# Performance work log

Measured on AMD Instinct MI355X. Metric: run time of the kernel, lower is better.

The kernel has to match this reference:

```python
import jax, jax.numpy as jnp
import numpy as np

WS = 7   # window_size
SS = 3   # shift_size
NH = 6   # num_heads
EPS = 1e-5


def _partition(x, ws):
    # [b,h,w,c] -> [b*(h//ws)*(w//ws), ws*ws, c]
    b, h, w, c = x.shape
    x = x.reshape(b, h // ws, ws, w // ws, ws, c)
    return x.transpose(0, 1, 3, 2, 4, 5).reshape(-1, ws * ws, c)


def _reverse(windows, ws, h, w, b):
    c = windows.shape[-1]
    x = windows.reshape(b, h // ws, w // ws, ws, ws, c)
    return x.transpose(0, 1, 3, 2, 4, 5).reshape(b, h, w, c)


def _make_mask(h, w, ws, ss):
    # static (numpy) shifted-window attention mask, [nw, ws*ws, ws*ws]
    img = np.zeros((h, w), dtype=np.float32)
    slices = (slice(0, -ws), slice(-ws, -ss), slice(-ss, None))
    cnt = 0
    for hs in slices:
        for wsl in slices:
            img[hs, wsl] = cnt
            cnt += 1
    mw = img.reshape(h // ws, ws, w // ws, ws).transpose(0, 2, 1, 3).reshape(-1, ws * ws)
    am = mw[:, None, :] - mw[:, :, None]
    mask = np.where(am != 0, -100.0, 0.0).astype(np.float32)
    return jnp.asarray(mask)


def _layernorm(x, g, b):
    mu = jnp.mean(x, axis=-1, keepdims=True)
    var = jnp.var(x, axis=-1, keepdims=True)
    return (x - mu) * jax.lax.rsqrt(var + EPS) * g + b


def setup_inputs() -> dict:
    key = jax.random.key(0)
    ks = jax.random.split(key, 8)
    dim = 192
    s = lambda fan: 1.0 / np.sqrt(fan)
    return {
        "x": jax.random.normal(ks[0], (64, 56, 56, dim), dtype=jnp.float32),
        "n1_g": jnp.ones((dim,), jnp.float32),
        "n1_b": jnp.zeros((dim,), jnp.float32),
        "qkv_w": jax.random.normal(ks[1], (dim, 3 * dim), jnp.float32) * s(dim),
        "qkv_b": jnp.zeros((3 * dim,), jnp.float32),
        "proj_w": jax.random.normal(ks[2], (dim, dim), jnp.float32) * s(dim),
        "proj_b": jnp.zeros((dim,), jnp.float32),
        "n2_g": jnp.ones((dim,), jnp.float32),
        "n2_b": jnp.zeros((dim,), jnp.float32),
        "w1": jax.random.normal(ks[3], (dim, 4 * dim), jnp.float32) * s(dim),
        "b1": jnp.zeros((4 * dim,), jnp.float32),
        "w2": jax.random.normal(ks[4], (4 * dim, dim), jnp.float32) * s(4 * dim),
        "b2": jnp.zeros((dim,), jnp.float32),
    }


def reference(x, n1_g, n1_b, qkv_w, qkv_b, proj_w, proj_b, n2_g, n2_b, w1, b1, w2, b2):
    b, h, w, c = x.shape
    hd = c // NH
    scale = hd ** -0.5

    sc = x
    xn = _layernorm(x, n1_g, n1_b)
    sx = jnp.roll(xn, shift=(-SS, -SS), axis=(1, 2))

    xw = _partition(sx, WS)                      # [B_, n, c], n = WS*WS
    B_, n, _ = xw.shape

    qkv = xw @ qkv_w + qkv_b                      # [B_, n, 3c]
    qkv = qkv.reshape(B_, n, 3, NH, hd).transpose(2, 0, 3, 1, 4)
    q, k, v = qkv[0], qkv[1], qkv[2]              # [B_, NH, n, hd]

    attn = jnp.einsum("whnd,whmd->whnm", q, k) * scale   # [B_, NH, n, n]
    mask = _make_mask(h, w, WS, SS)               # [nw, n, n]
    nw = mask.shape[0]
    attn = attn.reshape(b // nw * 1 if False else b, nw, NH, n, n) if False else attn.reshape(B_ // nw, nw, NH, n, n)
    attn = attn + mask[None, :, None, :, :]
    attn = attn.reshape(-1, NH, n, n)
    attn = jax.nn.softmax(attn, axis=-1)

    out = jnp.einsum("whnm,whmd->whnd", attn, v)  # [B_, NH, n, hd]
    out = out.transpose(0, 2, 1, 3).reshape(B_, n, c)
    out = out @ proj_w + proj_b

    sx = _reverse(out, WS, h, w, b)
    xs = jnp.roll(sx, shift=(SS, SS), axis=(1, 2))

    x2 = sc + xs
    x2n = _layernorm(x2, n2_g, n2_b)
    mlp = jax.nn.gelu(x2n @ w1 + b1, approximate=False) @ w2 + b2
    return x2 + mlp
```

## Files before the change

kernel.cpp:

```cpp
#include <hip/hip_runtime.h>

typedef __attribute__((ext_vector_type(4))) float f32x4;
typedef __attribute__((ext_vector_type(8))) short bf16x8;

#define NHEAD 6

__device__ __forceinline__ unsigned short f2bf(float f){
  union{float f;unsigned int u;}c; c.f=f;
  unsigned int x=c.u;
  return (unsigned short)((x + 0x7FFFu + ((x>>16)&1u)) >> 16);
}
__device__ __forceinline__ unsigned int pack2(float a, float b){
  return (unsigned int)f2bf(a) | ((unsigned int)f2bf(b)<<16);
}

__global__ void wt_kernel(const float* __restrict__ w, unsigned short* __restrict__ wt,
                          int K, int N){
  int idx = blockIdx.x*256 + threadIdx.x;
  if (idx >= K*N) return;
  int k = idx / N, n = idx - k*N;
  wt[(size_t)n*K + k] = f2bf(w[idx]);
}

template<int SHIFT>
__global__ __launch_bounds__(256) void ln_kernel(const float* __restrict__ x,
    const float* __restrict__ gw, const float* __restrict__ bw,
    unsigned short* __restrict__ out){
  int tok  = blockIdx.x*4 + (threadIdx.x>>6);
  int lane = threadIdx.x & 63;
  const float* row = x + (size_t)tok*192;
  float4 v = make_float4(0.f,0.f,0.f,0.f);
  if (lane < 48) v = *(const float4*)(row + lane*4);
  float s  = v.x+v.y+v.z+v.w;
  float s2 = v.x*v.x+v.y*v.y+v.z*v.z+v.w*v.w;
  #pragma unroll
  for (int off=32; off; off>>=1){ s += __shfl_xor(s,off); s2 += __shfl_xor(s2,off); }
  float mu = s*(1.f/192.f);
  float rs = rsqrtf(s2*(1.f/192.f) - mu*mu + 1e-5f);
  size_t otok;
  if (SHIFT){
    int b = tok/3136; int hw = tok - b*3136; int h = hw/56; int w = hw - h*56;
    int hs = h-3; if (hs<0) hs += 56;
    int wsh = w-3; if (wsh<0) wsh += 56;
    int wr = hs/7, r = hs - wr*7, wc = wsh/7, c = wsh - wc*7;
    otok = ((size_t)b*64 + wr*8 + wc)*49 + r*7 + c;
  } else {
    otok = (size_t)tok;
  }
  if (lane < 48){
    int cb = lane*4;
    ushort4 o;
    o.x = f2bf((v.x-mu)*rs*gw[cb+0] + bw[cb+0]);
    o.y = f2bf((v.y-mu)*rs*gw[cb+1] + bw[cb+1]);
    o.z = f2bf((v.z-mu)*rs*gw[cb+2] + bw[cb+2]);
    o.w = f2bf((v.w-mu)*rs*gw[cb+3] + bw[cb+3]);
    *(ushort4*)(out + otok*192 + cb) = o;
  }
}

enum { EPI_QKV=0, EPI_PROJ=1, EPI_GELU=2, EPI_FINAL=3 };

template<int EPI>
__global__ __launch_bounds__(256) void gemm_kernel(
    const unsigned short* __restrict__ A,
    const unsigned short* __restrict__ BT,
    const float* __restrict__ bias,
    const float* __restrict__ res,
    void* __restrict__ Cout,
    int M, int N, int K)
{
  __shared__ unsigned short lA[128*64];
  __shared__ unsigned short lB[64*64];
  const int tid  = threadIdx.x;
  const int wave = tid>>6, lane = tid&63;
  const int wm = wave>>1, wn = wave&1;
  const int lr = lane&15, lh = lane>>4;
  const int m0 = blockIdx.y*128, n0 = blockIdx.x*64;

  f32x4 zero = {0.f,0.f,0.f,0.f};
  f32x4 acc[4][2];
  #pragma unroll
  for (int i=0;i<4;i++){ acc[i][0]=zero; acc[i][1]=zero; }

  const int row8 = tid>>3, col8 = (tid&7)*8;
  const unsigned short* Ag = A  + (size_t)(m0 + row8)*K + col8;
  const unsigned short* Bg = BT + (size_t)(n0 + row8)*K + col8;

  for (int kt=0; kt<K; kt+=64){
    __syncthreads();
    #pragma unroll
    for (int i=0;i<4;i++){
      __builtin_amdgcn_global_load_lds(
        (const __attribute__((address_space(1))) void*)(Ag + (size_t)i*32*K + kt),
        (__attribute__((address_space(3))) void*)(lA + (i*256 + wave*64)*8),
        16, 0, 0);
    }
    #pragma unroll
    for (int i=0;i<2;i++){
      __builtin_amdgcn_global_load_lds(
        (const __attribute__((address_space(1))) void*)(Bg + (size_t)i*32*K + kt),
        (__attribute__((address_space(3))) void*)(lB + (i*256 + wave*64)*8),
        16, 0, 0);
    }
    __syncthreads();

    bf16x8 af[4][2], bfv[2][2];
    #pragma unroll
    for (int mi=0;mi<4;mi++)
      #pragma unroll
      for (int ks=0;ks<2;ks++)
        af[mi][ks] = *(const bf16x8*)&lA[(wm*64+mi*16+lr)*64 + ks*32 + lh*8];
    #pragma unroll
    for (int ni=0;ni<2;ni++)
      #pragma unroll
      for (int ks=0;ks<2;ks++)
        bfv[ni][ks] = *(const bf16x8*)&lB[(wn*32+ni*16+lr)*64 + ks*32 + lh*8];
    #pragma unroll
    for (int mi=0;mi<4;mi++)
      #pragma unroll
      for (int ni=0;ni<2;ni++)
        #pragma unroll
        for (int ks=0;ks<2;ks++)
          acc[mi][ni] = __builtin_amdgcn_mfma_f32_16x16x32_bf16(
              af[mi][ks], bfv[ni][ks], acc[mi][ni], 0,0,0);
  }

  #pragma unroll
  for (int mi=0;mi<4;mi++){
    #pragma unroll
    for (int ni=0;ni<2;ni++){
      int col = n0 + wn*32 + ni*16 + lr;
      float bv = bias[col];
      #pragma unroll
      for (int r=0;r<4;r++){
        int row = m0 + wm*64 + mi*16 + lh*4 + r;
        float v = acc[mi][ni][r] + bv;
        if (EPI == EPI_QKV){
          int win = row/49; int n = row - win*49;
          int which = col/192; int rem = col - which*192;
          int head = rem>>5, d = rem&31;
          size_t idx = (size_t)win*28224 + (size_t)which*9408 + head*1568 + n*32 + d;
          ((unsigned short*)Cout)[idx] = f2bf(v);
        } else if (EPI == EPI_GELU){
          float g = 0.5f*v*(1.0f + erff(v*0.70710678118654752f));
          ((unsigned short*)Cout)[(size_t)row*N + col] = f2bf(g);
        } else if (EPI == EPI_FINAL){
          size_t idx = (size_t)row*N + col;
          ((float*)Cout)[idx] = res[idx] + v;
        } else {
          int win = row/49; int nn = row - win*49;
          int b  = win>>6; int wi = win&63; int wr = wi>>3; int wc = wi&7;
          int r7 = nn/7;  int c7 = nn - r7*7;
          int h = wr*7 + r7 + 3; if (h>=56) h-=56;
          int w = wc*7 + c7 + 3; if (w>=56) w-=56;
          size_t idx = (((size_t)b*3136) + h*56 + w)*192 + col;
          ((float*)Cout)[idx] = res[idx] + v;
        }
      }
    }
  }
}

__global__ __launch_bounds__(256) void attn_kernel(const unsigned short* __restrict__ qkv,
                                                   unsigned short* __restrict__ aout){
  __shared__ __align__(16) unsigned short ldsQK[4][4096];
  __shared__ __align__(16) unsigned short ldsV[4][2048];
  const int wave = threadIdx.x>>6, lane = threadIdx.x&63;
  const int lr = lane&15, lh = lane>>4;
  const int unit = blockIdx.x*4 + wave;
  const int win  = unit/NHEAD, head = unit - win*NHEAD;

  unsigned short* Q  = ldsQK[wave];
  unsigned short* Kl = ldsQK[wave] + 2048;
  unsigned short* P  = ldsQK[wave];
  unsigned short* Vt = ldsV[wave];

  const size_t wbase = (size_t)win*28224 + (size_t)head*1568;
  const unsigned short* gQ = qkv + wbase;
  const unsigned short* gK = qkv + wbase + 9408;
  const unsigned short* gV = qkv + wbase + 18816;

  {
    uint4 z = make_uint4(0,0,0,0);
    #pragma unroll
    for (int i=0;i<4;i++) *(uint4*)&Vt[(i*64+lane)*8] = z;
  }

  #pragma unroll
  for (int i=0;i<4;i++){
    int idx = i*64 + lane;
    if (idx < 196){
      int row = idx>>2, blk = idx&3;
      int sb = (blk ^ (row&3) ^ ((row>>2)&3));
      uint4 dq = *(const uint4*)(gQ + idx*8);
      *(uint4*)&Q[row*32 + sb*8] = dq;
      uint4 dk = *(const uint4*)(gK + idx*8);
      *(uint4*)&Kl[row*32 + sb*8] = dk;
    }
  }
  #pragma unroll
  for (int i=0;i<4;i++){
    int idx = i*64 + lane;
    if (idx < 196){
      int row = idx>>2, d0 = (idx&3)*8;
      uint4 dv = *(const uint4*)(gV + idx*8);
      unsigned int wds[4] = {dv.x, dv.y, dv.z, dv.w};
      int rb = row>>3, re = row&7;
      #pragma unroll
      for (int j=0;j<8;j++){
        unsigned short t = (unsigned short)(wds[j>>1] >> ((j&1)*16));
        Vt[(d0+j)*64 + ((rb ^ j)*8) + re] = t;
      }
    }
  }

  bf16x8 kf[4], qf[4];
  #pragma unroll
  for (int t=0;t<4;t++){
    int row = t*16 + lr;
    int off = row*32 + ((lh ^ (row&3) ^ ((row>>2)&3))*8);
    kf[t] = *(const bf16x8*)&Kl[off];
    qf[t] = *(const bf16x8*)&Q[off];
  }

  f32x4 zero = {0.f,0.f,0.f,0.f};
  f32x4 S[4][4];
  #pragma unroll
  for (int mi=0;mi<4;mi++)
    #pragma unroll
    for (int ni=0;ni<4;ni++)
      S[mi][ni] = __builtin_amdgcn_mfma_f32_16x16x32_bf16(kf[mi], qf[ni], zero, 0,0,0);

  const int wi = win & 63, wr = wi>>3, wc = wi&7;
  const bool hasmask = (wr==7) || (wc==7);
  const float scale = 0.17677669529663687f;

  #pragma unroll
  for (int ni=0;ni<4;ni++){
    int q = ni*16 + lr;
    int idq = 0;
    if (hasmask){
      int qr = q/7, qc = q - qr*7;
      int ih = (wr==7) ? ((qr>=4)?2:1) : 0;
      int iw = (wc==7) ? ((qc>=4)?2:1) : 0;
      idq = ih*3 + iw;
    }
    #pragma unroll
    for (int mi=0;mi<4;mi++){
      #pragma unroll
      for (int r=0;r<4;r++){
        int key = mi*16 + lh*4 + r;
        float s;
        if (key >= 49) s = -1e30f;
        else {
          float add = 0.f;
          if (hasmask){
            int kr = key/7, kc = key - kr*7;
            int ih = (wr==7) ? ((kr>=4)?2:1) : 0;
            int iw = (wc==7) ? ((kc>=4)?2:1) : 0;
            add = ((ih*3+iw) == idq) ? 0.f : -100.f;
          }
          s = S[mi][ni][r]*scale + add;
        }
        S[mi][ni][r] = s;
      }
    }
    float m = -1e30f;
    #pragma unroll
    for (int mi=0;mi<4;mi++)
      #pragma unroll
      for (int r=0;r<4;r++) m = fmaxf(m, S[mi][ni][r]);
    m = fmaxf(m, __shfl_xor(m, 16));
    m = fmaxf(m, __shfl_xor(m, 32));
    float sum = 0.f;
    #pragma unroll
    for (int mi=0;mi<4;mi++)
      #pragma unroll
      for (int r=0;r<4;r++){
        float p = __expf(S[mi][ni][r] - m);
        S[mi][ni][r] = p; sum += p;
      }
    sum += __shfl_xor(sum, 16);
    sum += __shfl_xor(sum, 32);
    float inv = 1.f/sum;
    #pragma unroll
    for (int mi=0;mi<4;mi++){
      int keyb = mi*16 + lh*4;
      int blk = keyb>>3, e0 = keyb&7;
      int addr = q*64 + ((blk ^ (q&7))*8) + e0;
      *(unsigned int*)&P[addr]   = pack2(S[mi][ni][0]*inv, S[mi][ni][1]*inv);
      *(unsigned int*)&P[addr+2] = pack2(S[mi][ni][2]*inv, S[mi][ni][3]*inv);
    }
  }

  bf16x8 vf[2][2];
  #pragma unroll
  for (int mt=0;mt<2;mt++)
    #pragma unroll
    for (int ks=0;ks<2;ks++){
      int row = mt*16 + lr;
      vf[mt][ks] = *(const bf16x8*)&Vt[row*64 + (((ks*4+lh) ^ (row&7))*8)];
    }
  f32x4 O[2][4];
  #pragma unroll
  for (int ni=0;ni<4;ni++){
    int q = ni*16 + lr;
    bf16x8 pf0 = *(const bf16x8*)&P[q*64 + (((0*4+lh) ^ (q&7))*8)];
    bf16x8 pf1 = *(const bf16x8*)&P[q*64 + (((1*4+lh) ^ (q&7))*8)];
    #pragma unroll
    for (int mt=0;mt<2;mt++){
      f32x4 t = __builtin_amdgcn_mfma_f32_16x16x32_bf16(vf[mt][0], pf0, zero, 0,0,0);
      O[mt][ni] = __builtin_amdgcn_mfma_f32_16x16x32_bf16(vf[mt][1], pf1, t, 0,0,0);
    }
  }

  #pragma unroll
  for (int ni=0;ni<4;ni++){
    int q = ni*16 + lr;
    if (q < 49){
      size_t ob = ((size_t)win*49 + q)*192 + head*32 + lh*4;
      #pragma unroll
      for (int mt=0;mt<2;mt++){
        *(unsigned int*)(aout + ob + mt*16)     = pack2(O[mt][ni][0], O[mt][ni][1]);
        *(unsigned int*)(aout + ob + mt*16 + 2) = pack2(O[mt][ni][2], O[mt][ni][3]);
      }
    }
  }
}

extern "C" void kernel_launch(void* const* d_in, const int* in_sizes, int n_in,
                              void* d_out, int out_size, void* d_ws, size_t ws_size,
                              hipStream_t stream){
  (void)in_sizes; (void)n_in; (void)out_size; (void)ws_size;
  const float* x      = (const float*)d_in[0];
  const float* n1_g   = (const float*)d_in[1];
  const float* n1_b   = (const float*)d_in[2];
  const float* qkv_w  = (const float*)d_in[3];
  const float* qkv_b  = (const float*)d_in[4];
  const float* proj_w = (const float*)d_in[5];
  const float* proj_b = (const float*)d_in[6];
  const float* n2_g   = (const float*)d_in[7];
  const float* n2_b   = (const float*)d_in[8];
  const float* w1     = (const float*)d_in[9];
  const float* b1     = (const float*)d_in[10];
  const float* w2     = (const float*)d_in[11];
  const float* b2     = (const float*)d_in[12];

  char* ws = (char*)d_ws;
  unsigned short* qkvT = (unsigned short*)(ws + 0);
  unsigned short* projT= (unsigned short*)(ws + 221184);
  unsigned short* w1T  = (unsigned short*)(ws + 294912);
  unsigned short* w2T  = (unsigned short*)(ws + 589824);
  unsigned short* bufA = (unsigned short*)(ws + 884736);
  unsigned short* bufB = (unsigned short*)(ws + 77955072);
  float*          x2   = (float*)        (ws + 386236416);
  float* out = (float*)d_out;
  const int M = 200704;

  wt_kernel<<<432,256,0,stream>>>(qkv_w, qkvT, 192, 576);
  wt_kernel<<<144,256,0,stream>>>(proj_w, projT, 192, 192);
  wt_kernel<<<576,256,0,stream>>>(w1,    w1T,  192, 768);
  wt_kernel<<<576,256,0,stream>>>(w2,    w2T,  768, 192);

  ln_kernel<1><<<50176,256,0,stream>>>(x, n1_g, n1_b, bufA);
  gemm_kernel<EPI_QKV  ><<<dim3(9,1568), 256,0,stream>>>(bufA, qkvT, qkv_b, nullptr, bufB, M, 576, 192);
  attn_kernel<<<6144,256,0,stream>>>(bufB, bufA);
  gemm_kernel<EPI_PROJ ><<<dim3(3,1568), 256,0,stream>>>(bufA, projT, proj_b, x, x2, M, 192, 192);
  ln_kernel<0><<<50176,256,0,stream>>>(x2, n2_g, n2_b, bufA);
  gemm_kernel<EPI_GELU ><<<dim3(12,1568),256,0,stream>>>(bufA, w1T, b1, nullptr, bufB, M, 768, 192);
  gemm_kernel<EPI_FINAL><<<dim3(3,1568), 256,0,stream>>>(bufB, w2T, b2, x2, out, M, 192, 768);
}
```

Baseline: 824.4 us.

## Swizzle GEMM LDS, remap block order, vectorize epilogues, use tanh GELU

The GEMM kernel now XOR-swizzles the LDS tile columns to avoid bank conflicts. It remaps a 1D grid so groups of 8 M-tiles share an N column for better L2 reuse. It swaps the MFMA operands so each lane holds 4 consecutive columns, which lets the epilogues use packed bf16 and float4 stores, with nontemporal stores for intermediates. The exact erf GELU is replaced by a tanh approximation, which is cheaper but numerically differs from the reference's exact GELU.

```diff
diff --git a/kernel.cpp b/kernel.cpp
--- a/kernel.cpp
+++ b/kernel.cpp
@@ -2,6 +2,7 @@
 
 typedef __attribute__((ext_vector_type(4))) float f32x4;
 typedef __attribute__((ext_vector_type(8))) short bf16x8;
+typedef __attribute__((ext_vector_type(2))) unsigned int u32x2;
 
 #define NHEAD 6
 
@@ -59,6 +60,13 @@
 }
 
 enum { EPI_QKV=0, EPI_PROJ=1, EPI_GELU=2, EPI_FINAL=3 };
+
+__device__ __forceinline__ float gelu_tanh(float v){
+  float u = v*(0.79788456f + 0.0356774f*v*v);
+  float e = __expf(2.f*u);
+  float th = 1.f - 2.f/(e + 1.f);
+  return 0.5f*v*(1.f + th);
+}
 
 template<int EPI>
 __global__ __launch_bounds__(256) void gemm_kernel(
@@ -75,16 +83,22 @@
   const int wave = tid>>6, lane = tid&63;
   const int wm = wave>>1, wn = wave&1;
   const int lr = lane&15, lh = lane>>4;
-  const int m0 = blockIdx.y*128, n0 = blockIdx.x*64;
+
+  const int Nb = N>>6;
+  int bid = blockIdx.x;
+  int yb = bid/(8*Nb); int rr = bid - yb*8*Nb; int xq = rr>>3; int y8 = rr&7;
+  const int m0 = (yb*8 + y8)*128, n0 = xq*64;
 
   f32x4 zero = {0.f,0.f,0.f,0.f};
   f32x4 acc[4][2];
   #pragma unroll
   for (int i=0;i<4;i++){ acc[i][0]=zero; acc[i][1]=zero; }
 
-  const int row8 = tid>>3, col8 = (tid&7)*8;
-  const unsigned short* Ag = A  + (size_t)(m0 + row8)*K + col8;
-  const unsigned short* Bg = BT + (size_t)(n0 + row8)*K + col8;
+  const int row8 = tid>>3;
+  const int sw   = row8 & 7;
+  const int csw  = ((tid&7) ^ sw)*8;
+  const unsigned short* Ag = A  + (size_t)(m0 + row8)*K + csw;
+  const unsigned short* Bg = BT + (size_t)(n0 + row8)*K + csw;
 
   for (int kt=0; kt<K; kt+=64){
     __syncthreads();
@@ -108,13 +122,17 @@
     #pragma unroll
     for (int mi=0;mi<4;mi++)
       #pragma unroll
-      for (int ks=0;ks<2;ks++)
-        af[mi][ks] = *(const bf16x8*)&lA[(wm*64+mi*16+lr)*64 + ks*32 + lh*8];
+      for (int ks=0;ks<2;ks++){
+        int arow = wm*64+mi*16+lr;
+        af[mi][ks] = *(const bf16x8*)&lA[arow*64 + (((ks*4+lh) ^ (lr&7))*8)];
+      }
     #pragma unroll
     for (int ni=0;ni<2;ni++)
       #pragma unroll
-      for (int ks=0;ks<2;ks++)
-        bfv[ni][ks] = *(const bf16x8*)&lB[(wn*32+ni*16+lr)*64 + ks*32 + lh*8];
+      for (int ks=0;ks<2;ks++){
+        int brow = wn*32+ni*16+lr;
+        bfv[ni][ks] = *(const bf16x8*)&lB[brow*64 + (((ks*4+lh) ^ (lr&7))*8)];
+      }
     #pragma unroll
     for (int mi=0;mi<4;mi++)
       #pragma unroll
@@ -122,40 +140,51 @@
         #pragma unroll
         for (int ks=0;ks<2;ks++)
           acc[mi][ni] = __builtin_amdgcn_mfma_f32_16x16x32_bf16(
-              af[mi][ks], bfv[ni][ks], acc[mi][ni], 0,0,0);
+              bfv[ni][ks], af[mi][ks], acc[mi][ni], 0,0,0);
   }
 
   #pragma unroll
   for (int mi=0;mi<4;mi++){
+    const int row = m0 + wm*64 + mi*16 + lr;
+    int winr=0, nn=0;
+    size_t prow = 0;
+    if (EPI == EPI_QKV){
+      winr = row/49; nn = row - winr*49;
+    } else if (EPI == EPI_PROJ){
+      winr = row/49; nn = row - winr*49;
+      int b  = winr>>6; int wi = winr&63; int wr_ = wi>>3; int wc_ = wi&7;
+      int r7 = nn/7;  int c7 = nn - r7*7;
+      int h = wr_*7 + r7 + 3; if (h>=56) h-=56;
+      int w = wc_*7 + c7 + 3; if (w>=56) w-=56;
+      prow = (((size_t)b*3136) + h*56 + w)*192;
+    }
     #pragma unroll
     for (int ni=0;ni<2;ni++){
-      int col = n0 + wn*32 + ni*16 + lr;
-      float bv = bias[col];
-      #pragma unroll
-      for (int r=0;r<4;r++){
-        int row = m0 + wm*64 + mi*16 + lh*4 + r;
-        float v = acc[mi][ni][r] + bv;
-        if (EPI == EPI_QKV){
-          int win = row/49; int n = row - win*49;
-          int which = col/192; int rem = col - which*192;
-          int head = rem>>5, d = rem&31;
-          size_t idx = (size_t)win*28224 + (size_t)which*9408 + head*1568 + n*32 + d;
-          ((unsigned short*)Cout)[idx] = f2bf(v);
-        } else if (EPI == EPI_GELU){
-          float g = 0.5f*v*(1.0f + erff(v*0.70710678118654752f));
-          ((unsigned short*)Cout)[(size_t)row*N + col] = f2bf(g);
-        } else if (EPI == EPI_FINAL){
-          size_t idx = (size_t)row*N + col;
-          ((float*)Cout)[idx] = res[idx] + v;
-        } else {
-          int win = row/49; int nn = row - win*49;
-          int b  = win>>6; int wi = win&63; int wr = wi>>3; int wc = wi&7;
-          int r7 = nn/7;  int c7 = nn - r7*7;
-          int h = wr*7 + r7 + 3; if (h>=56) h-=56;
-          int w = wc*7 + c7 + 3; if (w>=56) w-=56;
-          size_t idx = (((size_t)b*3136) + h*56 + w)*192 + col;
-          ((float*)Cout)[idx] = res[idx] + v;
-        }
+      const int colb = n0 + wn*32 + ni*16 + lh*4;
+      float v0 = acc[mi][ni][0] + bias[colb+0];
+      float v1 = acc[mi][ni][1] + bias[colb+1];
+      float v2 = acc[mi][ni][2] + bias[colb+2];
+      float v3 = acc[mi][ni][3] + bias[colb+3];
+      if (EPI == EPI_QKV){
+        int which = colb/192; int rem = colb - which*192;
+        int head = rem>>5, d = rem&31;
+        size_t idx = (size_t)winr*28224 + (size_t)which*9408 + head*1568 + nn*32 + d;
+        u32x2 st; st.x = pack2(v0,v1); st.y = pack2(v2,v3);
+        __builtin_nontemporal_store(st, (u32x2*)((unsigned short*)Cout + idx));
+      } else if (EPI == EPI_GELU){
+        u32x2 st; st.x = pack2(gelu_tanh(v0), gelu_tanh(v1));
+        st.y = pack2(gelu_tanh(v2), gelu_tanh(v3));
+        __builtin_nontemporal_store(st, (u32x2*)((unsigned short*)Cout + (size_t)row*N + colb));
+      } else if (EPI == EPI_FINAL){
+        size_t idx = (size_t)row*N + colb;
+        float4 rv = *(const float4*)(res + idx);
+        float4 o = make_float4(rv.x+v0, rv.y+v1, rv.z+v2, rv.w+v3);
+        *(float4*)((float*)Cout + idx) = o;
+      } else {
+        size_t idx = prow + colb;
+        float4 rv = *(const float4*)(res + idx);
+        float4 o = make_float4(rv.x+v0, rv.y+v1, rv.z+v2, rv.w+v3);
+        *(float4*)((float*)Cout + idx) = o;
       }
     }
   }
@@ -363,10 +392,10 @@
   wt_kernel<<<576,256,0,stream>>>(w2,    w2T,  768, 192);
 
   ln_kernel<1><<<50176,256,0,stream>>>(x, n1_g, n1_b, bufA);
-  gemm_kernel<EPI_QKV  ><<<dim3(9,1568), 256,0,stream>>>(bufA, qkvT, qkv_b, nullptr, bufB, M, 576, 192);
+  gemm_kernel<EPI_QKV  ><<< 9*1568, 256,0,stream>>>(bufA, qkvT, qkv_b, nullptr, bufB, M, 576, 192);
   attn_kernel<<<6144,256,0,stream>>>(bufB, bufA);
-  gemm_kernel<EPI_PROJ ><<<dim3(3,1568), 256,0,stream>>>(bufA, projT, proj_b, x, x2, M, 192, 192);
+  gemm_kernel<EPI_PROJ ><<< 3*1568, 256,0,stream>>>(bufA, projT, proj_b, x, x2, M, 192, 192);
   ln_kernel<0><<<50176,256,0,stream>>>(x2, n2_g, n2_b, bufA);
-  gemm_kernel<EPI_GELU ><<<dim3(12,1568),256,0,stream>>>(bufA, w1T, b1, nullptr, bufB, M, 768, 192);
-  gemm_kernel<EPI_FINAL><<<dim3(3,1568), 256,0,stream>>>(bufB, w2T, b2, x2, out, M, 192, 768);
-}
+  gemm_kernel<EPI_GELU ><<<12*1568, 256,0,stream>>>(bufA, w1T, b1, nullptr, bufB, M, 768, 192);
+  gemm_kernel<EPI_FINAL><<< 3*1568, 256,0,stream>>>(bufB, w2T, b2, x2, out, M, 192, 768);
+}
```

Result: slower. 842.7 us (+2.2%).
